# Kernel tuning notes

Hardware: AMD Instinct MI355X
Metric: run time of the kernel (lower is better)

Reference implementation:

```python
import jax, jax.numpy as jnp
import numpy as np

D_MODEL = 1024
D_STATE = 16
D_CONV = 4
D_INNER = 2048  # expand * d_model
BATCH = 2
LENGTH = 2048


def silu(u):
    return u * jax.nn.sigmoid(u)


def setup_inputs() -> dict:
    key = jax.random.key(0)
    ks = jax.random.split(key, 8)
    sc = 0.02
    x = jax.random.normal(ks[0], (BATCH, LENGTH, D_MODEL), jnp.float32)
    W_in = jax.random.normal(ks[1], (2 * D_INNER, D_MODEL), jnp.float32) * sc
    conv_w = jax.random.normal(ks[2], (D_INNER, 1, D_CONV), jnp.float32) * 0.1
    conv_b = jnp.zeros((D_INNER,), jnp.float32)
    W_x = jax.random.normal(ks[3], (D_INNER + 2 * D_STATE, D_INNER), jnp.float32) * sc
    W_dt = jax.random.normal(ks[4], (D_INNER, D_INNER), jnp.float32) * sc
    b_dt = jnp.zeros((D_INNER,), jnp.float32)
    # A = arange(1, d_state+1) repeated for each inner channel (per source init)
    A_log = jnp.log(jnp.tile(jnp.arange(1, D_STATE + 1, dtype=jnp.float32), (D_INNER, 1)))
    D = jnp.ones((D_INNER,), jnp.float32)
    W_out = jax.random.normal(ks[5], (D_MODEL, D_INNER), jnp.float32) * sc
    ln_g = jnp.ones((D_MODEL,), jnp.float32)
    ln_b = jnp.zeros((D_MODEL,), jnp.float32)
    return dict(x=x, W_in=W_in, conv_w=conv_w, conv_b=conv_b, W_x=W_x, W_dt=W_dt,
                b_dt=b_dt, A_log=A_log, D=D, W_out=W_out, ln_g=ln_g, ln_b=ln_b)


def reference(x, W_in, conv_w, conv_b, W_x, W_dt, b_dt, A_log, D, W_out, ln_g, ln_b):
    b, l, _ = x.shape
    residual = x
    # in_proj, split into x-path and gate z
    xz = x @ W_in.T  # (b, l, 2*d_inner)
    xs, z = jnp.split(xz, 2, axis=-1)
    # depthwise causal conv1d (left pad d_conv-1, take first l outputs)
    xc = jnp.transpose(xs, (0, 2, 1))  # (b, d_inner, l)
    xc = jax.lax.conv_general_dilated(
        xc, conv_w, window_strides=(1,), padding=[(D_CONV - 1, 0)],
        dimension_numbers=('NCH', 'OIH', 'NCH'), feature_group_count=D_INNER)
    xc = xc + conv_b[None, :, None]
    u = silu(jnp.transpose(xc, (0, 2, 1)))  # (b, l, d_inner)
    # SSM parameter projection
    proj = u @ W_x.T  # (b, l, d_inner + 2*d_state)
    d_in, Bm, Cm = jnp.split(proj, [D_INNER, D_INNER + D_STATE], axis=-1)
    delta = jax.nn.softplus(d_in @ W_dt.T + b_dt)  # (b, l, d_inner)
    A = -jnp.exp(A_log)  # (d_inner, d_state)
    dA = jnp.exp(delta[..., None] * A)                         # (b, l, d, n)
    dBu = delta[..., None] * Bm[:, :, None, :] * u[..., None]  # (b, l, d, n)

    def step(state, inp):
        dA_t, dBu_t, c_t = inp
        state = state * dA_t + dBu_t            # (b, d, n)
        y_t = jnp.einsum('bdn,bn->bd', state, c_t)
        return state, y_t

    init = jnp.zeros((b, D_INNER, D_STATE), x.dtype)
    _, ys = jax.lax.scan(step, init, (jnp.transpose(dA, (1, 0, 2, 3)),
                                      jnp.transpose(dBu, (1, 0, 2, 3)),
                                      jnp.transpose(Cm, (1, 0, 2))))
    y = jnp.transpose(ys, (1, 0, 2)) + u * D  # (b, l, d_inner)
    y = y * silu(z)
    out = y @ W_out.T + residual
    mu = jnp.mean(out, axis=-1, keepdims=True)
    var = jnp.var(out, axis=-1, keepdims=True)
    return (out - mu) / jnp.sqrt(var + 1e-5) * ln_g + ln_b
```

## Files before the change

### kernel.cpp

```cpp
#include <hip/hip_runtime.h>

typedef unsigned short u16;
typedef unsigned int u32;
typedef __bf16 bf16x8_t __attribute__((ext_vector_type(8)));
typedef float f32x4_t __attribute__((ext_vector_type(4)));


#define NCH 64
#define CLEN 32

__device__ __forceinline__ u16 f2bf(float f) {
  u32 u = __float_as_uint(f);
  return (u16)((u + 0x7fffu + ((u >> 16) & 1u)) >> 16);
}
__device__ __forceinline__ float bf2f(u16 h) { return __uint_as_float(((u32)h) << 16); }

__device__ __forceinline__ void async_ld16(const u16* g, u16* l) {
  __builtin_amdgcn_global_load_lds((const __attribute__((address_space(1))) void*)g,
                                   (__attribute__((address_space(3))) void*)l, 16, 0, 0);
}

__global__ void k_cvt(const float* __restrict__ in, u16* __restrict__ out, int n4) {
  int g = blockIdx.x * 256 + threadIdx.x;
  if (g >= n4) return;
  float4 v = reinterpret_cast<const float4*>(in)[g];
  u32 lo = (u32)f2bf(v.x) | ((u32)f2bf(v.y) << 16);
  u32 hi = (u32)f2bf(v.z) | ((u32)f2bf(v.w) << 16);
  reinterpret_cast<uint2*>(out)[g] = make_uint2(lo, hi);
}

__global__ void k_cvt_pad(const float* __restrict__ in, u16* __restrict__ out,
                          int n4_valid, int n4_total) {
  int g = blockIdx.x * 256 + threadIdx.x;
  if (g >= n4_total) return;
  u32 lo = 0, hi = 0;
  if (g < n4_valid) {
    float4 v = reinterpret_cast<const float4*>(in)[g];
    lo = (u32)f2bf(v.x) | ((u32)f2bf(v.y) << 16);
    hi = (u32)f2bf(v.z) | ((u32)f2bf(v.w) << 16);
  }
  reinterpret_cast<uint2*>(out)[g] = make_uint2(lo, hi);
}

template <bool WB, bool WF>
__global__ __launch_bounds__(256, 2) void k_gemm_bt(
    const u16* __restrict__ A, int lda, const u16* __restrict__ B, int ldb,
    float* __restrict__ Cf, int fcol0, int ldcf,
    u16* __restrict__ Cb, int ldc, int K) {
  __shared__ __align__(16) u16 sA[128 * 64];
  __shared__ __align__(16) u16 sB[128 * 64];
  const int tid = threadIdx.x;
  const int lane = tid & 63;
  const int wave = tid >> 6;
  const size_t tm = (size_t)blockIdx.y * 128;
  const size_t tn = (size_t)blockIdx.x * 128;
  const int wm = (wave & 1) * 64;
  const int wn = (wave >> 1) * 64;
  const int mrow = lane & 15;
  const int quad = lane >> 4;

  f32x4_t acc[4][4];
#pragma unroll
  for (int i = 0; i < 4; ++i)
#pragma unroll
    for (int j = 0; j < 4; ++j) {
      acc[i][j][0] = 0.f; acc[i][j][1] = 0.f; acc[i][j][2] = 0.f; acc[i][j][3] = 0.f;
    }

  for (int k0 = 0; k0 < K; k0 += 64) {
#pragma unroll
    for (int j = 0; j < 4; ++j) {
      int idx = j * 256 + tid;
      int row = idx >> 3;
      int col = (idx & 7) << 3;
      async_ld16(A + (tm + row) * (size_t)lda + (k0 + col), sA + (size_t)idx * 8);
      async_ld16(B + (tn + row) * (size_t)ldb + (k0 + col), sB + (size_t)idx * 8);
    }
    __syncthreads();
#pragma unroll
    for (int kk = 0; kk < 64; kk += 32) {
      bf16x8_t af[4], bfr[4];
#pragma unroll
      for (int i = 0; i < 4; ++i)
        af[i] = *reinterpret_cast<const bf16x8_t*>(sA + (wm + i * 16 + mrow) * 64 + kk + quad * 8);
#pragma unroll
      for (int i = 0; i < 4; ++i)
        bfr[i] = *reinterpret_cast<const bf16x8_t*>(sB + (wn + i * 16 + mrow) * 64 + kk + quad * 8);
#pragma unroll
      for (int i = 0; i < 4; ++i)
#pragma unroll
        for (int j = 0; j < 4; ++j)
          acc[i][j] = __builtin_amdgcn_mfma_f32_16x16x32_bf16(af[i], bfr[j], acc[i][j], 0, 0, 0);
    }
    __syncthreads();
  }

#pragma unroll
  for (int i = 0; i < 4; ++i)
#pragma unroll
    for (int j = 0; j < 4; ++j) {
      size_t r0 = tm + wm + i * 16 + quad * 4;
      size_t c = tn + wn + j * 16 + mrow;
#pragma unroll
      for (int r = 0; r < 4; ++r) {
        float v = acc[i][j][r];
        if (WF && (int)c >= fcol0) Cf[(r0 + r) * (size_t)ldcf + (c - fcol0)] = v;
        if (WB) Cb[(r0 + r) * (size_t)ldc + c] = f2bf(v);
      }
    }
}

__global__ void k_conv_silu(const u16* __restrict__ xz, const float* __restrict__ cw,
                            const float* __restrict__ cb, u16* __restrict__ u) {
  int g = blockIdx.x * 256 + threadIdx.x;
  int d = g & 2047;
  int l = (g >> 11) & 2047;
  int b = g >> 22;
  float acc = cb[d];
#pragma unroll
  for (int k = 0; k < 4; ++k) {
    int lp = l + k - 3;
    if (lp >= 0) acc += bf2f(xz[((size_t)(b * 2048 + lp) << 12) + d]) * cw[d * 4 + k];
  }
  float s = acc / (1.f + __expf(-acc));
  u[g] = f2bf(s);
}

__device__ __forceinline__ float softplus_fast(float x) {
  return __logf(1.f + __expf(x));
}

__global__ void k_scan1(const u16* __restrict__ dpre, const float* __restrict__ bdt,
                        const u16* __restrict__ u, const float* __restrict__ projBC,
                        const float* __restrict__ A_log, float* __restrict__ sF,
                        float* __restrict__ aF) {
  int d = blockIdx.x * 256 + threadIdx.x;
  int c = blockIdx.y, b = blockIdx.z;
  float A[16], s[16], ap[16];
#pragma unroll
  for (int q = 0; q < 4; ++q) {
    float4 al = reinterpret_cast<const float4*>(A_log + d * 16)[q];
    A[q * 4 + 0] = -__expf(al.x); A[q * 4 + 1] = -__expf(al.y);
    A[q * 4 + 2] = -__expf(al.z); A[q * 4 + 3] = -__expf(al.w);
  }
#pragma unroll
  for (int n = 0; n < 16; ++n) { s[n] = 0.f; ap[n] = 1.f; }
  float bd = bdt[d];
  int t0 = c * CLEN;
  for (int t = t0; t < t0 + CLEN; ++t) {
    size_t rb = (size_t)(b * 2048 + t);
    float delta = softplus_fast(bf2f(dpre[rb * 2048 + d]) + bd);
    float du = delta * bf2f(u[rb * 2048 + d]);
    const float4* Bp = reinterpret_cast<const float4*>(projBC + rb * 128);
    float4 B0 = Bp[0], B1 = Bp[1], B2 = Bp[2], B3 = Bp[3];
    float Bv[16] = {B0.x, B0.y, B0.z, B0.w, B1.x, B1.y, B1.z, B1.w,
                    B2.x, B2.y, B2.z, B2.w, B3.x, B3.y, B3.z, B3.w};
#pragma unroll
    for (int n = 0; n < 16; ++n) {
      float dA = __expf(delta * A[n]);
      s[n] = fmaf(s[n], dA, du * Bv[n]);
      ap[n] *= dA;
    }
  }
  size_t o = ((size_t)((b * NCH + c) * 2048 + d)) << 4;
#pragma unroll
  for (int q = 0; q < 4; ++q) {
    reinterpret_cast<float4*>(sF + o)[q] = make_float4(s[q * 4], s[q * 4 + 1], s[q * 4 + 2], s[q * 4 + 3]);
    reinterpret_cast<float4*>(aF + o)[q] = make_float4(ap[q * 4], ap[q * 4 + 1], ap[q * 4 + 2], ap[q * 4 + 3]);
  }
}

__global__ void k_scan_carry(const float* __restrict__ sF, const float* __restrict__ aF,
                             float* __restrict__ carry) {
  int g = blockIdx.x * 256 + threadIdx.x;
  int b = g >> 15;
  int dn = g & 32767;
  float S = 0.f;
#pragma unroll 4
  for (int c = 0; c < NCH; ++c) {
    size_t idx = ((size_t)(b * NCH + c) << 15) + dn;
    carry[idx] = S;
    S = S * aF[idx] + sF[idx];
  }
}

__global__ void k_scan3(const u16* __restrict__ dpre, const float* __restrict__ bdt,
                        const u16* __restrict__ u, const float* __restrict__ projBC,
                        const float* __restrict__ A_log, const float* __restrict__ carry,
                        const float* __restrict__ Dvec, const u16* __restrict__ xz,
                        u16* __restrict__ ybf) {
  int d = blockIdx.x * 256 + threadIdx.x;
  int c = blockIdx.y, b = blockIdx.z;
  float A[16], s[16];
#pragma unroll
  for (int q = 0; q < 4; ++q) {
    float4 al = reinterpret_cast<const float4*>(A_log + d * 16)[q];
    A[q * 4 + 0] = -__expf(al.x); A[q * 4 + 1] = -__expf(al.y);
    A[q * 4 + 2] = -__expf(al.z); A[q * 4 + 3] = -__expf(al.w);
  }
  size_t o = ((size_t)((b * NCH + c) * 2048 + d)) << 4;
#pragma unroll
  for (int q = 0; q < 4; ++q) {
    float4 cv = reinterpret_cast<const float4*>(carry + o)[q];
    s[q * 4] = cv.x; s[q * 4 + 1] = cv.y; s[q * 4 + 2] = cv.z; s[q * 4 + 3] = cv.w;
  }
  float bd = bdt[d];
  float Dd = Dvec[d];
  int t0 = c * CLEN;
  for (int t = t0; t < t0 + CLEN; ++t) {
    size_t rb = (size_t)(b * 2048 + t);
    float delta = softplus_fast(bf2f(dpre[rb * 2048 + d]) + bd);
    float uv = bf2f(u[rb * 2048 + d]);
    float du = delta * uv;
    const float4* Bp = reinterpret_cast<const float4*>(projBC + rb * 128);
    float4 B0 = Bp[0], B1 = Bp[1], B2 = Bp[2], B3 = Bp[3];
    float4 C0 = Bp[4], C1 = Bp[5], C2 = Bp[6], C3 = Bp[7];
    float Bv[16] = {B0.x, B0.y, B0.z, B0.w, B1.x, B1.y, B1.z, B1.w,
                    B2.x, B2.y, B2.z, B2.w, B3.x, B3.y, B3.z, B3.w};
    float Cv[16] = {C0.x, C0.y, C0.z, C0.w, C1.x, C1.y, C1.z, C1.w,
                    C2.x, C2.y, C2.z, C2.w, C3.x, C3.y, C3.z, C3.w};
    float yv = 0.f;
#pragma unroll
    for (int n = 0; n < 16; ++n) {
      float dA = __expf(delta * A[n]);
      s[n] = fmaf(s[n], dA, du * Bv[n]);
      yv = fmaf(s[n], Cv[n], yv);
    }
    yv += uv * Dd;
    float z = bf2f(xz[(rb << 12) + 2048 + d]);
    yv *= z / (1.f + __expf(-z));
    ybf[rb * 2048 + d] = f2bf(yv);
  }
}

__global__ void k_ln(const float* __restrict__ pre, const float* __restrict__ x,
                     const float* __restrict__ gam, const float* __restrict__ bet,
                     float* __restrict__ out) {
  int row = blockIdx.x, tid = threadIdx.x;
  size_t base = (size_t)row * 1024 + tid * 4;
  float4 v = *reinterpret_cast<const float4*>(pre + base);
  float4 r = *reinterpret_cast<const float4*>(x + base);
  v.x += r.x; v.y += r.y; v.z += r.z; v.w += r.w;
  float s = v.x + v.y + v.z + v.w;
  float s2 = v.x * v.x + v.y * v.y + v.z * v.z + v.w * v.w;
#pragma unroll
  for (int o = 32; o >= 1; o >>= 1) {
    s += __shfl_xor(s, o);
    s2 += __shfl_xor(s2, o);
  }
  __shared__ float red[8];
  int lane = tid & 63, wv = tid >> 6;
  if (lane == 0) { red[wv] = s; red[4 + wv] = s2; }
  __syncthreads();
  s = red[0] + red[1] + red[2] + red[3];
  s2 = red[4] + red[5] + red[6] + red[7];
  float mu = s * (1.f / 1024.f);
  float var = s2 * (1.f / 1024.f) - mu * mu;
  float rstd = rsqrtf(var + 1e-5f);
  float4 gg = *reinterpret_cast<const float4*>(gam + tid * 4);
  float4 bb = *reinterpret_cast<const float4*>(bet + tid * 4);
  float4 o;
  o.x = (v.x - mu) * rstd * gg.x + bb.x;
  o.y = (v.y - mu) * rstd * gg.y + bb.y;
  o.z = (v.z - mu) * rstd * gg.z + bb.z;
  o.w = (v.w - mu) * rstd * gg.w + bb.w;
  *reinterpret_cast<float4*>(out + base) = o;
}

extern "C" void kernel_launch(void* const* d_in, const int* in_sizes, int n_in,
                              void* d_out, int out_size, void* d_ws, size_t ws_size,
                              hipStream_t stream) {
  (void)in_sizes; (void)n_in; (void)out_size; (void)ws_size;
  const float* x = (const float*)d_in[0];
  const float* W_in = (const float*)d_in[1];
  const float* conv_w = (const float*)d_in[2];
  const float* conv_b = (const float*)d_in[3];
  const float* W_x = (const float*)d_in[4];
  const float* W_dt = (const float*)d_in[5];
  const float* b_dt = (const float*)d_in[6];
  const float* A_log = (const float*)d_in[7];
  const float* Dv = (const float*)d_in[8];
  const float* W_out = (const float*)d_in[9];
  const float* ln_g = (const float*)d_in[10];
  const float* ln_b = (const float*)d_in[11];
  float* out = (float*)d_out;

  char* p = (char*)d_ws;
  u16* xz_bf = (u16*)p;      p += (size_t)4096 * 4096 * 2;
  u16* u_bf = (u16*)p;       p += (size_t)4096 * 2048 * 2;
  float* projBC = (float*)p; p += (size_t)4096 * 128 * 4;
  u16* projbf = (u16*)p;     p += (size_t)4096 * 2176 * 2;
  u16* dpre_bf = (u16*)p;    p += (size_t)4096 * 2048 * 2;
  u16* ybf = (u16*)p;        p += (size_t)4096 * 2048 * 2;
  float* sF = (float*)p;     p += (size_t)2 * NCH * 2048 * 16 * 4;
  float* aF = (float*)p;     p += (size_t)2 * NCH * 2048 * 16 * 4;
  float* carry = (float*)p;  p += (size_t)2 * NCH * 2048 * 16 * 4;
  u16* Wx_bf = (u16*)p;      p += (size_t)2176 * 2048 * 2;
  u16* Wdt_bf = (u16*)p;     p += (size_t)2048 * 2048 * 2;
  u16* Wout_bf = (u16*)p;    p += (size_t)1024 * 2048 * 2;
  u16* x_bf = (u16*)p;       p += (size_t)4096 * 1024 * 2;
  u16* Win_bf = (u16*)p;     p += (size_t)4096 * 1024 * 2;
  float* outpre = (float*)x_bf;

  k_cvt<<<4096, 256, 0, stream>>>(x, x_bf, 1048576);
  k_cvt<<<4096, 256, 0, stream>>>(W_in, Win_bf, 1048576);
  k_cvt_pad<<<4352, 256, 0, stream>>>(W_x, Wx_bf, 1064960, 1114112);
  k_cvt<<<4096, 256, 0, stream>>>(W_dt, Wdt_bf, 1048576);
  k_cvt<<<2048, 256, 0, stream>>>(W_out, Wout_bf, 524288);

  k_gemm_bt<true, false><<<dim3(32, 32), 256, 0, stream>>>(
      x_bf, 1024, Win_bf, 1024, nullptr, 0, 0, xz_bf, 4096, 1024);
  k_conv_silu<<<32768, 256, 0, stream>>>(xz_bf, conv_w, conv_b, u_bf);
  k_gemm_bt<true, true><<<dim3(17, 32), 256, 0, stream>>>(
      u_bf, 2048, Wx_bf, 2048, projBC, 2048, 128, projbf, 2176, 2048);
  k_gemm_bt<true, false><<<dim3(16, 32), 256, 0, stream>>>(
      projbf, 2176, Wdt_bf, 2048, nullptr, 0, 0, dpre_bf, 2048, 2048);
  k_scan1<<<dim3(8, NCH, 2), 256, 0, stream>>>(dpre_bf, b_dt, u_bf, projBC, A_log, sF, aF);
  k_scan_carry<<<256, 256, 0, stream>>>(sF, aF, carry);
  k_scan3<<<dim3(8, NCH, 2), 256, 0, stream>>>(dpre_bf, b_dt, u_bf, projBC, A_log, carry,
                                               Dv, xz_bf, ybf);
  k_gemm_bt<false, true><<<dim3(8, 32), 256, 0, stream>>>(
      ybf, 2048, Wout_bf, 2048, outpre, 0, 1024, nullptr, 0, 2048);
  k_ln<<<4096, 256, 0, stream>>>(outpre, x, ln_g, ln_b, out);
}
```

Measured before the change: 484.1 us.

## Double-buffer GEMM LDS, split-K out-proj, and fuse weight conversions

Merges the five fp32-to-bf16 conversion launches into one kernel that dispatches on the global index. Adds an optional double-buffered LDS path to the bf16 GEMM so the next K tile is loaded asynchronously while MFMAs run on the current one. This path is enabled for the x-projection, dt and out-projection GEMMs. The out-projection also gets a 2-way split-K over blockIdx.z, which doubles its block count. The two fp32 partials go into the scan scratch buffer and are summed in the layernorm kernel. Double buffering doubles LDS per block, which may lower occupancy, and split-K adds extra fp32 traffic.

```diff
diff --git a/kernel.cpp b/kernel.cpp
--- a/kernel.cpp
+++ b/kernel.cpp
@@ -20,40 +20,44 @@
                                    (__attribute__((address_space(3))) void*)l, 16, 0, 0);
 }
 
-__global__ void k_cvt(const float* __restrict__ in, u16* __restrict__ out, int n4) {
+__global__ void k_cvt_all(const float* __restrict__ x, u16* __restrict__ x_bf,
+                          const float* __restrict__ W_in, u16* __restrict__ Win_bf,
+                          const float* __restrict__ W_x, u16* __restrict__ Wx_bf,
+                          const float* __restrict__ W_dt, u16* __restrict__ Wdt_bf,
+                          const float* __restrict__ W_out, u16* __restrict__ Wout_bf) {
   int g = blockIdx.x * 256 + threadIdx.x;
-  if (g >= n4) return;
-  float4 v = reinterpret_cast<const float4*>(in)[g];
-  u32 lo = (u32)f2bf(v.x) | ((u32)f2bf(v.y) << 16);
-  u32 hi = (u32)f2bf(v.z) | ((u32)f2bf(v.w) << 16);
-  reinterpret_cast<uint2*>(out)[g] = make_uint2(lo, hi);
-}
-
-__global__ void k_cvt_pad(const float* __restrict__ in, u16* __restrict__ out,
-                          int n4_valid, int n4_total) {
-  int g = blockIdx.x * 256 + threadIdx.x;
-  if (g >= n4_total) return;
+  const float* src;
+  u16* dst;
+  int rel;
+  bool valid = true;
+  if (g < 1048576) { src = x; dst = x_bf; rel = g; }
+  else if (g < 2097152) { src = W_in; dst = Win_bf; rel = g - 1048576; }
+  else if (g < 3211264) { src = W_x; dst = Wx_bf; rel = g - 2097152; valid = rel < 1064960; }
+  else if (g < 4259840) { src = W_dt; dst = Wdt_bf; rel = g - 3211264; }
+  else if (g < 4784128) { src = W_out; dst = Wout_bf; rel = g - 4259840; }
+  else return;
   u32 lo = 0, hi = 0;
-  if (g < n4_valid) {
-    float4 v = reinterpret_cast<const float4*>(in)[g];
+  if (valid) {
+    float4 v = reinterpret_cast<const float4*>(src)[rel];
     lo = (u32)f2bf(v.x) | ((u32)f2bf(v.y) << 16);
     hi = (u32)f2bf(v.z) | ((u32)f2bf(v.w) << 16);
   }
-  reinterpret_cast<uint2*>(out)[g] = make_uint2(lo, hi);
-}
-
-template <bool WB, bool WF>
+  reinterpret_cast<uint2*>(dst)[rel] = make_uint2(lo, hi);
+}
+
+template <bool WB, bool WF, bool DB>
 __global__ __launch_bounds__(256, 2) void k_gemm_bt(
     const u16* __restrict__ A, int lda, const u16* __restrict__ B, int ldb,
-    float* __restrict__ Cf, int fcol0, int ldcf,
+    float* __restrict__ Cf, int fcol0, int ldcf, size_t fsplit,
     u16* __restrict__ Cb, int ldc, int K) {
-  __shared__ __align__(16) u16 sA[128 * 64];
-  __shared__ __align__(16) u16 sB[128 * 64];
+  __shared__ __align__(16) u16 sA[(DB ? 2 : 1) * 128 * 64];
+  __shared__ __align__(16) u16 sB[(DB ? 2 : 1) * 128 * 64];
   const int tid = threadIdx.x;
   const int lane = tid & 63;
   const int wave = tid >> 6;
   const size_t tm = (size_t)blockIdx.y * 128;
   const size_t tn = (size_t)blockIdx.x * 128;
+  const int kbase = blockIdx.z * K;
   const int wm = (wave & 1) * 64;
   const int wn = (wave >> 1) * 64;
   const int mrow = lane & 15;
@@ -67,34 +71,55 @@
       acc[i][j][0] = 0.f; acc[i][j][1] = 0.f; acc[i][j][2] = 0.f; acc[i][j][3] = 0.f;
     }
 
-  for (int k0 = 0; k0 < K; k0 += 64) {
+  auto stage = [&](int k0, int buf) {
 #pragma unroll
     for (int j = 0; j < 4; ++j) {
       int idx = j * 256 + tid;
       int row = idx >> 3;
       int col = (idx & 7) << 3;
-      async_ld16(A + (tm + row) * (size_t)lda + (k0 + col), sA + (size_t)idx * 8);
-      async_ld16(B + (tn + row) * (size_t)ldb + (k0 + col), sB + (size_t)idx * 8);
-    }
-    __syncthreads();
+      async_ld16(A + (tm + row) * (size_t)lda + (kbase + k0 + col), sA + buf * 8192 + (size_t)idx * 8);
+      async_ld16(B + (tn + row) * (size_t)ldb + (kbase + k0 + col), sB + buf * 8192 + (size_t)idx * 8);
+    }
+  };
+  auto compute = [&](int buf) {
+    const u16* bA = sA + buf * 8192;
+    const u16* bB = sB + buf * 8192;
 #pragma unroll
     for (int kk = 0; kk < 64; kk += 32) {
       bf16x8_t af[4], bfr[4];
 #pragma unroll
       for (int i = 0; i < 4; ++i)
-        af[i] = *reinterpret_cast<const bf16x8_t*>(sA + (wm + i * 16 + mrow) * 64 + kk + quad * 8);
+        af[i] = *reinterpret_cast<const bf16x8_t*>(bA + (wm + i * 16 + mrow) * 64 + kk + quad * 8);
 #pragma unroll
       for (int i = 0; i < 4; ++i)
-        bfr[i] = *reinterpret_cast<const bf16x8_t*>(sB + (wn + i * 16 + mrow) * 64 + kk + quad * 8);
+        bfr[i] = *reinterpret_cast<const bf16x8_t*>(bB + (wn + i * 16 + mrow) * 64 + kk + quad * 8);
 #pragma unroll
       for (int i = 0; i < 4; ++i)
 #pragma unroll
         for (int j = 0; j < 4; ++j)
           acc[i][j] = __builtin_amdgcn_mfma_f32_16x16x32_bf16(af[i], bfr[j], acc[i][j], 0, 0, 0);
     }
+  };
+
+  if (DB) {
+    const int nit = K >> 6;
+    stage(0, 0);
     __syncthreads();
-  }
-
+    for (int it = 0; it < nit; ++it) {
+      if (it + 1 < nit) stage((it + 1) << 6, (it + 1) & 1);
+      compute(it & 1);
+      __syncthreads();
+    }
+  } else {
+    for (int k0 = 0; k0 < K; k0 += 64) {
+      stage(k0, 0);
+      __syncthreads();
+      compute(0);
+      __syncthreads();
+    }
+  }
+
+  if (WF) Cf += (size_t)blockIdx.z * fsplit;
 #pragma unroll
   for (int i = 0; i < 4; ++i)
 #pragma unroll
@@ -239,8 +264,9 @@
   int row = blockIdx.x, tid = threadIdx.x;
   size_t base = (size_t)row * 1024 + tid * 4;
   float4 v = *reinterpret_cast<const float4*>(pre + base);
+  float4 p1 = *reinterpret_cast<const float4*>(pre + 4194304 + base);
   float4 r = *reinterpret_cast<const float4*>(x + base);
-  v.x += r.x; v.y += r.y; v.z += r.z; v.w += r.w;
+  v.x += p1.x + r.x; v.y += p1.y + r.y; v.z += p1.z + r.z; v.w += p1.w + r.w;
   float s = v.x + v.y + v.z + v.w;
   float s2 = v.x * v.x + v.y * v.y + v.z * v.z + v.w * v.w;
 #pragma unroll
@@ -300,26 +326,23 @@
   u16* Wout_bf = (u16*)p;    p += (size_t)1024 * 2048 * 2;
   u16* x_bf = (u16*)p;       p += (size_t)4096 * 1024 * 2;
   u16* Win_bf = (u16*)p;     p += (size_t)4096 * 1024 * 2;
-  float* outpre = (float*)x_bf;
-
-  k_cvt<<<4096, 256, 0, stream>>>(x, x_bf, 1048576);
-  k_cvt<<<4096, 256, 0, stream>>>(W_in, Win_bf, 1048576);
-  k_cvt_pad<<<4352, 256, 0, stream>>>(W_x, Wx_bf, 1064960, 1114112);
-  k_cvt<<<4096, 256, 0, stream>>>(W_dt, Wdt_bf, 1048576);
-  k_cvt<<<2048, 256, 0, stream>>>(W_out, Wout_bf, 524288);
-
-  k_gemm_bt<true, false><<<dim3(32, 32), 256, 0, stream>>>(
-      x_bf, 1024, Win_bf, 1024, nullptr, 0, 0, xz_bf, 4096, 1024);
+  float* outpre = sF;
+
+  k_cvt_all<<<18688, 256, 0, stream>>>(x, x_bf, W_in, Win_bf, W_x, Wx_bf, W_dt, Wdt_bf,
+                                       W_out, Wout_bf);
+
+  k_gemm_bt<true, false, false><<<dim3(32, 32), 256, 0, stream>>>(
+      x_bf, 1024, Win_bf, 1024, nullptr, 0, 0, 0, xz_bf, 4096, 1024);
   k_conv_silu<<<32768, 256, 0, stream>>>(xz_bf, conv_w, conv_b, u_bf);
-  k_gemm_bt<true, true><<<dim3(17, 32), 256, 0, stream>>>(
-      u_bf, 2048, Wx_bf, 2048, projBC, 2048, 128, projbf, 2176, 2048);
-  k_gemm_bt<true, false><<<dim3(16, 32), 256, 0, stream>>>(
-      projbf, 2176, Wdt_bf, 2048, nullptr, 0, 0, dpre_bf, 2048, 2048);
+  k_gemm_bt<true, true, true><<<dim3(17, 32), 256, 0, stream>>>(
+      u_bf, 2048, Wx_bf, 2048, projBC, 2048, 128, 0, projbf, 2176, 2048);
+  k_gemm_bt<true, false, true><<<dim3(16, 32), 256, 0, stream>>>(
+      projbf, 2176, Wdt_bf, 2048, nullptr, 0, 0, 0, dpre_bf, 2048, 2048);
   k_scan1<<<dim3(8, NCH, 2), 256, 0, stream>>>(dpre_bf, b_dt, u_bf, projBC, A_log, sF, aF);
   k_scan_carry<<<256, 256, 0, stream>>>(sF, aF, carry);
   k_scan3<<<dim3(8, NCH, 2), 256, 0, stream>>>(dpre_bf, b_dt, u_bf, projBC, A_log, carry,
                                                Dv, xz_bf, ybf);
-  k_gemm_bt<false, true><<<dim3(8, 32), 256, 0, stream>>>(
-      ybf, 2048, Wout_bf, 2048, outpre, 0, 1024, nullptr, 0, 2048);
+  k_gemm_bt<false, true, true><<<dim3(8, 32, 2), 256, 0, stream>>>(
+      ybf, 2048, Wout_bf, 2048, outpre, 0, 1024, (size_t)4096 * 1024, nullptr, 0, 1024);
   k_ln<<<4096, 256, 0, stream>>>(outpre, x, ln_g, ln_b, out);
 }
```

New measurement: 483.2 us. About the same (-0.2%).
